# Kernel tuning notes

Measured on AMD Instinct MI355X. Metric: run time of the kernel, lower is better.

## Reference

```python
import jax, jax.numpy as jnp
import numpy as np

B, L, H, NH = 2, 512, 128, 2
DH = H // NH
POS_VOCAB, REL_VOCAB = 512, 257


def setup_inputs() -> dict:
    key = jax.random.key(0)
    ks = jax.random.split(key, 16)
    s = 0.02
    inp = {
        "query": jax.random.normal(ks[0], (B, L, H), jnp.float32),
        "key": jax.random.normal(ks[1], (B, L, H), jnp.float32),
        "value": jax.random.normal(ks[2], (B, L, H), jnp.float32),
        "Wq": jax.random.normal(ks[3], (H, H), jnp.float32) * s,
        "bq": jnp.zeros((H,), jnp.float32),
        "Wk": jax.random.normal(ks[4], (H, H), jnp.float32) * s,
        "bk": jnp.zeros((H,), jnp.float32),
        "Wv": jax.random.normal(ks[5], (H, H), jnp.float32) * s,
        "bv": jnp.zeros((H,), jnp.float32),
        "Wo": jax.random.normal(ks[6], (H, H), jnp.float32) * s,
        "bo": jnp.zeros((H,), jnp.float32),
        "E_PK": jax.random.normal(ks[7], (POS_VOCAB, H), jnp.float32) * s,
        "E_PV": jax.random.normal(ks[8], (POS_VOCAB, H), jnp.float32) * s,
        "E_RK": jax.random.normal(ks[9], (REL_VOCAB, H), jnp.float32) * s,
        "E_RV": jax.random.normal(ks[10], (REL_VOCAB, H), jnp.float32) * s,
        "poss_seq": jax.random.randint(ks[11], (B, L), 0, POS_VOCAB),
        "interval_seq": jax.random.randint(ks[12], (B, L, L), 0, REL_VOCAB),
        # causal mask (True = attend), same role as attn_mask in the torch module
        "attn_mask": jnp.broadcast_to(jnp.tril(jnp.ones((L, L), bool)), (B, L, L)),
    }
    return inp


def reference(query, key, value, Wq, bq, Wk, bk, Wv, bv, Wo, bo,
              E_PK, E_PV, E_RK, E_RV, poss_seq, interval_seq, attn_mask):
    b, l, _ = query.shape
    # linear projections (torch Linear: x @ W.T + b)
    Q = query @ Wq.T + bq
    K = key @ Wk.T + bk + E_PK[poss_seq]
    V = value @ Wv.T + bv + E_PV[poss_seq]
    # relative key/value embeddings: (b, l, l, h, dh) -> (b, h, l, l, dh)
    rel_k = E_RK[interval_seq].reshape(b, l, l, NH, DH).transpose(0, 3, 1, 2, 4)
    rel_v = E_RV[interval_seq].reshape(b, l, l, NH, DH).transpose(0, 3, 1, 2, 4)
    # split heads: (b, h, l, dh)
    Qh = Q.reshape(b, l, NH, DH).transpose(0, 2, 1, 3)
    Kh = K.reshape(b, l, NH, DH).transpose(0, 2, 1, 3)
    Vh = V.reshape(b, l, NH, DH).transpose(0, 2, 1, 3)
    scores = jnp.einsum('bhld,bhkd->bhlk', Qh, Kh)
    scores = scores + jnp.einsum('bhld,bhlkd->bhlk', Qh, rel_k)
    scores = scores / jnp.sqrt(jnp.float32(DH))
    m = attn_mask[:, None]  # (b, 1, l, l)
    scores = jnp.where(m, scores, -jnp.inf)
    w = jax.nn.softmax(scores, axis=-1)
    w = jnp.where(m, w, 0.0)
    out = jnp.einsum('bhlk,bhkd->bhld', w, Vh)
    out = out + jnp.einsum('bhlk,bhlkd->bhld', w, rel_v)
    out = out.transpose(0, 2, 1, 3).reshape(b, l, H)
    out = out @ Wo.T + bo
    out = jnp.where(jnp.isnan(out), 0.0, out)
    return out
```

## Files before the change

kernel.cpp:

```cpp
#include <hip/hip_runtime.h>
#include <math.h>

#define LL 512
#define HH 128
#define NHH 2
#define DHH 64
#define RELV 257

#define OFF_QH   0
#define OFF_KT   131072
#define OFF_VH   262144
#define OFF_PK   393216
#define OFF_WQT  919552
#define OFF_WKT  935936
#define OFF_WVT  952320
#define OFF_WOT  968704
#define OFF_ERKT 985088

__global__ void prep_kernel(const float* Wq, const float* Wk, const float* Wv,
                            const float* Wo, const float* E_RK, float* ws) {
    int g = blockIdx.x * 256 + threadIdx.x;
    if (g < 65536) {
        int m = g >> 14, rem = g & 16383, i = rem >> 7, j = rem & 127;
        const float* W = (m == 0) ? Wq : (m == 1) ? Wk : (m == 2) ? Wv : Wo;
        ws[OFF_WQT + m * 16384 + i * 128 + j] = W[j * 128 + i];
    } else if (g < 65536 + 128 * RELV) {
        int g2 = g - 65536;
        int hd = g2 / RELV, r = g2 - hd * RELV;
        ws[OFF_ERKT + hd * RELV + r] = E_RK[r * HH + hd];
    }
}

__launch_bounds__(256)
__global__ void qkv_kernel(const float* q_in, const float* k_in, const float* v_in,
                           const float* bq, const float* bk, const float* bv,
                           const float* E_PK, const float* E_PV, const int* poss,
                           const float* Wqt, const float* Wkt, const float* Wvt,
                           const float* ERKt,
                           float* Qh, float* Kt, float* Vh, float* PK) {
    int row0 = blockIdx.x * 2;
    int b = row0 >> 9;
    int l0 = row0 & 511;
    int t = threadIdx.x;

    __shared__ float xin[3][2][128];
    __shared__ float pp[3][2][2][128];
    __shared__ float qr[2][128];

    for (int g = t; g < 768; g += 256) {
        int m = g >> 8, rem = g & 255, rr = rem >> 7, i = rem & 127;
        const float* src = (m == 0) ? q_in : (m == 1) ? k_in : v_in;
        xin[m][rr][i] = src[(row0 + rr) * 128 + i];
    }
    __syncthreads();

    int j = t & 127, half = t >> 7;
    float aq0 = 0, ak0 = 0, av0 = 0, aq1 = 0, ak1 = 0, av1 = 0;
    int i0 = half * 64;
#pragma unroll 8
    for (int i = i0; i < i0 + 64; i++) {
        float wq = Wqt[i * 128 + j], wk = Wkt[i * 128 + j], wv = Wvt[i * 128 + j];
        aq0 += xin[0][0][i] * wq; aq1 += xin[0][1][i] * wq;
        ak0 += xin[1][0][i] * wk; ak1 += xin[1][1][i] * wk;
        av0 += xin[2][0][i] * wv; av1 += xin[2][1][i] * wv;
    }
    pp[0][0][half][j] = aq0; pp[0][1][half][j] = aq1;
    pp[1][0][half][j] = ak0; pp[1][1][half][j] = ak1;
    pp[2][0][half][j] = av0; pp[2][1][half][j] = av1;
    __syncthreads();

    {
        int rr = t >> 7;
        int row = row0 + rr, l = l0 + rr;
        int pos = poss[row];
        float q = pp[0][rr][0][j] + pp[0][rr][1][j] + bq[j];
        float k = pp[1][rr][0][j] + pp[1][rr][1][j] + bk[j] + E_PK[pos * 128 + j];
        float v = pp[2][rr][0][j] + pp[2][rr][1][j] + bv[j] + E_PV[pos * 128 + j];
        int h = j >> 6, d = j & 63, bh = b * NHH + h;
        Qh[(bh * LL + l) * DHH + d] = q;
        Vh[(bh * LL + l) * DHH + d] = v;
        Kt[(bh * DHH + d) * LL + l] = k;
        qr[rr][j] = q;
    }
    __syncthreads();

    int h = t >> 7, rl = t & 127;
    const float* qh0 = qr[0] + h * 64;
    const float* qh1 = qr[1] + h * 64;
    const float* erb = ERKt + h * 64 * RELV;
    float* pk0 = PK + ((b * NHH + h) * LL + l0) * RELV;
    float* pk1 = pk0 + RELV;
#pragma unroll
    for (int pass = 0; pass < 3; pass++) {
        int r = rl + pass * 128;
        if (r < RELV) {
            float a0 = 0.f, a1 = 0.f;
#pragma unroll 8
            for (int dd = 0; dd < 64; dd++) {
                float er = erb[dd * RELV + r];
                a0 += qh0[dd] * er; a1 += qh1[dd] * er;
            }
            pk0[r] = a0; pk1[r] = a1;
        }
    }
}

__launch_bounds__(512)
__global__ void attn_kernel(const float* Qh, const float* Kt, const float* Vh,
                            const float* PK, const float* E_RV,
                            const float* Wot, const float* bo,
                            const int* interval, float* out) {
    int blk = blockIdx.x;
    int b = blk & 1;
    int l = 511 - (blk >> 1);
    int t = threadIdx.x;
    int w = t >> 6, lane = t & 63;
    int h = w >> 2, s = w & 3;
    int bh = b * NHH + h;
    int nk = l + 1;
    int kstep = (((nk + 3) >> 2) + 1) & ~1;
    int kbase = s * kstep; if (kbase > nk) kbase = nk;
    int kend = kbase + kstep; if (kend > nk) kend = nk;

    __shared__ float q2[2][DHH];
    __shared__ float pks[2][RELV];
    __shared__ float wb[2][RELV];
    __shared__ __align__(8) float sc[8][128];
    __shared__ float oa[8][DHH];
    __shared__ float ao[HH];
    __shared__ float po[4][HH];
    __shared__ float reds[8];

    if (t < 128) {
        int hh = t >> 6, dd = t & 63;
        q2[hh][dd] = Qh[((b * NHH + hh) * LL + l) * DHH + dd];
    }
    for (int idx = t; idx < 2 * RELV; idx += 512) {
        int hh = idx >= RELV;
        int r = idx - hh * RELV;
        pks[hh][r] = PK[((b * NHH + hh) * LL + l) * RELV + r];
        wb[hh][r] = 0.f;
    }
    __syncthreads();

    int k0 = kbase + lane * 2;
    const int* idxr = interval + (b * LL + l) * LL;
    float ax = 0.f, ay = 0.f;
    int2 i2 = make_int2(0, 0);
    if (k0 < kend) {
        i2 = *(const int2*)(idxr + k0);
        const float* kb = Kt + bh * DHH * LL + k0;
#pragma unroll 16
        for (int d = 0; d < DHH; d++) {
            float2 kk = *(const float2*)(kb + d * LL);
            float qd = q2[h][d];
            ax += qd * kk.x; ay += qd * kk.y;
        }
    }
    float e0 = (k0 + 0 < kend) ? __expf((ax + pks[h][i2.x]) * 0.125f) : 0.f;
    float e1 = (k0 + 1 < kend) ? __expf((ay + pks[h][i2.y]) * 0.125f) : 0.f;

    float ssum = e0 + e1;
#pragma unroll
    for (int off = 32; off > 0; off >>= 1) ssum += __shfl_down(ssum, off);
    if (lane == 0) reds[w] = ssum;

    *(float2*)&sc[w][lane * 2] = make_float2(e0, e1);
    if (k0 + 0 < kend) atomicAdd(&wb[h][i2.x], e0);
    if (k0 + 1 < kend) atomicAdd(&wb[h][i2.y], e1);
    __syncthreads();

    float acc0 = 0.f, acc1 = 0.f, acc2 = 0.f, acc3 = 0.f;
    const float* vb = Vh + bh * LL * DHH + lane;
    int kcnt = kend - kbase; if (kcnt < 0) kcnt = 0;
    int niter = (kcnt + 3) >> 2;
    for (int ci = 0; ci < niter; ci++) {
        int k = kbase + ci * 4;
        const float* scw = sc[w] + ci * 4;
        acc0 += scw[0] * vb[(k + 0) * DHH];
        acc1 += scw[1] * vb[(k + 1) * DHH];
        acc2 += scw[2] * vb[(k + 2) * DHH];
        acc3 += scw[3] * vb[(k + 3) * DHH];
    }

    {
        int r0 = s * 64;
        const float* ev = E_RV + h * 64 + lane;
        const float* wbh = wb[h];
#pragma unroll 4
        for (int rr = 0; rr < 64; rr += 4) {
            int r = r0 + rr;
            acc0 += wbh[r + 0] * ev[(r + 0) * HH];
            acc1 += wbh[r + 1] * ev[(r + 1) * HH];
            acc2 += wbh[r + 2] * ev[(r + 2) * HH];
            acc3 += wbh[r + 3] * ev[(r + 3) * HH];
        }
        if (s == 3) acc0 += wbh[256] * ev[256 * HH];
    }

    float inv = 1.f / (((reds[h * 4 + 0] + reds[h * 4 + 1]) +
                        (reds[h * 4 + 2] + reds[h * 4 + 3])));
    oa[w][lane] = ((acc0 + acc1) + (acc2 + acc3)) * inv;
    __syncthreads();

    if (t < 128) {
        int hh = t >> 6, dd = t & 63;
        ao[t] = (oa[hh * 4 + 0][dd] + oa[hh * 4 + 1][dd]) +
                (oa[hh * 4 + 2][dd] + oa[hh * 4 + 3][dd]);
    }
    __syncthreads();

    int j = t & 127, iq = t >> 7;
    float pa = 0.f, pb = 0.f;
    int ib = iq * 32;
#pragma unroll 8
    for (int ii = 0; ii < 32; ii += 2) {
        pa += ao[ib + ii]     * Wot[(ib + ii) * HH + j];
        pb += ao[ib + ii + 1] * Wot[(ib + ii + 1) * HH + j];
    }
    po[iq][j] = pa + pb;
    __syncthreads();
    if (t < HH) {
        float o = (po[0][t] + po[1][t]) + (po[2][t] + po[3][t]) + bo[t];
        if (isnan(o)) o = 0.f;
        out[(b * LL + l) * HH + t] = o;
    }
}

extern "C" void kernel_launch(void* const* d_in, const int* in_sizes, int n_in,
                              void* d_out, int out_size, void* d_ws, size_t ws_size,
                              hipStream_t stream) {
    const float* query = (const float*)d_in[0];
    const float* key   = (const float*)d_in[1];
    const float* value = (const float*)d_in[2];
    const float* Wq = (const float*)d_in[3];  const float* bq = (const float*)d_in[4];
    const float* Wk = (const float*)d_in[5];  const float* bk = (const float*)d_in[6];
    const float* Wv = (const float*)d_in[7];  const float* bv = (const float*)d_in[8];
    const float* Wo = (const float*)d_in[9];  const float* bo = (const float*)d_in[10];
    const float* E_PK = (const float*)d_in[11];
    const float* E_PV = (const float*)d_in[12];
    const float* E_RK = (const float*)d_in[13];
    const float* E_RV = (const float*)d_in[14];
    const int* poss     = (const int*)d_in[15];
    const int* interval = (const int*)d_in[16];

    float* ws = (float*)d_ws;
    float* Qh   = ws + OFF_QH;
    float* Kt   = ws + OFF_KT;
    float* Vh   = ws + OFF_VH;
    float* PK   = ws + OFF_PK;
    float* Wqt  = ws + OFF_WQT;
    float* Wkt  = ws + OFF_WKT;
    float* Wvt  = ws + OFF_WVT;
    float* Wot  = ws + OFF_WOT;
    float* ERKt = ws + OFF_ERKT;
    float* out = (float*)d_out;

    prep_kernel<<<385, 256, 0, stream>>>(Wq, Wk, Wv, Wo, E_RK, ws);
    qkv_kernel<<<512, 256, 0, stream>>>(query, key, value, bq, bk, bv,
                                        E_PK, E_PV, poss, Wqt, Wkt, Wvt, ERKt,
                                        Qh, Kt, Vh, PK);
    attn_kernel<<<1024, 512, 0, stream>>>(Qh, Kt, Vh, PK, E_RV, Wot, bo,
                                          interval, out);
}
```

Measured before the change: 140.8 us.

## Fuse prep, QKV and attention kernels into one cooperative persistent kernel

Replaces the three kernel launches with one cooperative kernel that uses grid-wide syncs between the weight-transpose, projection/PK and attention phases. Blocks loop over rows persistently, with the grid sized from an occupancy query. This removes launch gaps and inter-kernel drain. In exchange it adds grid.sync overhead, a host occupancy query on every call, and a QKV phase that now handles one row per block iteration instead of two, so each weight load is reused less.

```diff
diff --git a/kernel.cpp b/kernel.cpp
--- a/kernel.cpp
+++ b/kernel.cpp
@@ -1,5 +1,8 @@
 #include <hip/hip_runtime.h>
+#include <hip/hip_cooperative_groups.h>
 #include <math.h>
+
+namespace cg = cooperative_groups;
 
 #define LL 512
 #define HH 128
@@ -17,111 +20,46 @@
 #define OFF_WOT  968704
 #define OFF_ERKT 985088
 
-__global__ void prep_kernel(const float* Wq, const float* Wk, const float* Wv,
-                            const float* Wo, const float* E_RK, float* ws) {
-    int g = blockIdx.x * 256 + threadIdx.x;
-    if (g < 65536) {
-        int m = g >> 14, rem = g & 16383, i = rem >> 7, j = rem & 127;
-        const float* W = (m == 0) ? Wq : (m == 1) ? Wk : (m == 2) ? Wv : Wo;
-        ws[OFF_WQT + m * 16384 + i * 128 + j] = W[j * 128 + i];
-    } else if (g < 65536 + 128 * RELV) {
-        int g2 = g - 65536;
-        int hd = g2 / RELV, r = g2 - hd * RELV;
-        ws[OFF_ERKT + hd * RELV + r] = E_RK[r * HH + hd];
+__global__ void fused_kernel(const float* q_in, const float* k_in, const float* v_in,
+                             const float* bq, const float* bk, const float* bv,
+                             const float* Wq, const float* Wk, const float* Wv,
+                             const float* Wo, const float* bo,
+                             const float* E_PK, const float* E_PV,
+                             const float* E_RK, const float* E_RV,
+                             const int* poss, const int* interval,
+                             float* ws, float* out) {
+    cg::grid_group grid = cg::this_grid();
+    int t = threadIdx.x;
+
+    float* Qh   = ws + OFF_QH;
+    float* Kt   = ws + OFF_KT;
+    float* Vh   = ws + OFF_VH;
+    float* PK   = ws + OFF_PK;
+    float* Wt   = ws + OFF_WQT;
+    float* ERKt = ws + OFF_ERKT;
+
+    for (int g = blockIdx.x * 512 + t; g < 65536 + 128 * RELV;
+         g += gridDim.x * 512) {
+        if (g < 65536) {
+            int m = g >> 14, rem = g & 16383, i = rem >> 7, j = rem & 127;
+            const float* W = (m == 0) ? Wq : (m == 1) ? Wk : (m == 2) ? Wv : Wo;
+            Wt[m * 16384 + i * 128 + j] = W[j * 128 + i];
+        } else {
+            int g2 = g - 65536;
+            int hd = g2 / RELV, r = g2 - hd * RELV;
+            ERKt[hd * RELV + r] = E_RK[r * HH + hd];
+        }
     }
-}
-
-__launch_bounds__(256)
-__global__ void qkv_kernel(const float* q_in, const float* k_in, const float* v_in,
-                           const float* bq, const float* bk, const float* bv,
-                           const float* E_PK, const float* E_PV, const int* poss,
-                           const float* Wqt, const float* Wkt, const float* Wvt,
-                           const float* ERKt,
-                           float* Qh, float* Kt, float* Vh, float* PK) {
-    int row0 = blockIdx.x * 2;
-    int b = row0 >> 9;
-    int l0 = row0 & 511;
-    int t = threadIdx.x;
-
-    __shared__ float xin[3][2][128];
-    __shared__ float pp[3][2][2][128];
-    __shared__ float qr[2][128];
-
-    for (int g = t; g < 768; g += 256) {
-        int m = g >> 8, rem = g & 255, rr = rem >> 7, i = rem & 127;
-        const float* src = (m == 0) ? q_in : (m == 1) ? k_in : v_in;
-        xin[m][rr][i] = src[(row0 + rr) * 128 + i];
-    }
-    __syncthreads();
-
-    int j = t & 127, half = t >> 7;
-    float aq0 = 0, ak0 = 0, av0 = 0, aq1 = 0, ak1 = 0, av1 = 0;
-    int i0 = half * 64;
-#pragma unroll 8
-    for (int i = i0; i < i0 + 64; i++) {
-        float wq = Wqt[i * 128 + j], wk = Wkt[i * 128 + j], wv = Wvt[i * 128 + j];
-        aq0 += xin[0][0][i] * wq; aq1 += xin[0][1][i] * wq;
-        ak0 += xin[1][0][i] * wk; ak1 += xin[1][1][i] * wk;
-        av0 += xin[2][0][i] * wv; av1 += xin[2][1][i] * wv;
-    }
-    pp[0][0][half][j] = aq0; pp[0][1][half][j] = aq1;
-    pp[1][0][half][j] = ak0; pp[1][1][half][j] = ak1;
-    pp[2][0][half][j] = av0; pp[2][1][half][j] = av1;
-    __syncthreads();
-
-    {
-        int rr = t >> 7;
-        int row = row0 + rr, l = l0 + rr;
-        int pos = poss[row];
-        float q = pp[0][rr][0][j] + pp[0][rr][1][j] + bq[j];
-        float k = pp[1][rr][0][j] + pp[1][rr][1][j] + bk[j] + E_PK[pos * 128 + j];
-        float v = pp[2][rr][0][j] + pp[2][rr][1][j] + bv[j] + E_PV[pos * 128 + j];
-        int h = j >> 6, d = j & 63, bh = b * NHH + h;
-        Qh[(bh * LL + l) * DHH + d] = q;
-        Vh[(bh * LL + l) * DHH + d] = v;
-        Kt[(bh * DHH + d) * LL + l] = k;
-        qr[rr][j] = q;
-    }
-    __syncthreads();
-
-    int h = t >> 7, rl = t & 127;
-    const float* qh0 = qr[0] + h * 64;
-    const float* qh1 = qr[1] + h * 64;
-    const float* erb = ERKt + h * 64 * RELV;
-    float* pk0 = PK + ((b * NHH + h) * LL + l0) * RELV;
-    float* pk1 = pk0 + RELV;
-#pragma unroll
-    for (int pass = 0; pass < 3; pass++) {
-        int r = rl + pass * 128;
-        if (r < RELV) {
-            float a0 = 0.f, a1 = 0.f;
-#pragma unroll 8
-            for (int dd = 0; dd < 64; dd++) {
-                float er = erb[dd * RELV + r];
-                a0 += qh0[dd] * er; a1 += qh1[dd] * er;
-            }
-            pk0[r] = a0; pk1[r] = a1;
-        }
-    }
-}
-
-__launch_bounds__(512)
-__global__ void attn_kernel(const float* Qh, const float* Kt, const float* Vh,
-                            const float* PK, const float* E_RV,
-                            const float* Wot, const float* bo,
-                            const int* interval, float* out) {
-    int blk = blockIdx.x;
-    int b = blk & 1;
-    int l = 511 - (blk >> 1);
-    int t = threadIdx.x;
-    int w = t >> 6, lane = t & 63;
-    int h = w >> 2, s = w & 3;
-    int bh = b * NHH + h;
-    int nk = l + 1;
-    int kstep = (((nk + 3) >> 2) + 1) & ~1;
-    int kbase = s * kstep; if (kbase > nk) kbase = nk;
-    int kend = kbase + kstep; if (kend > nk) kend = nk;
-
+    grid.sync();
+
+    const float* Wqt = Wt;
+    const float* Wkt = Wt + 16384;
+    const float* Wvt = Wt + 32768;
+    const float* Wot = Wt + 49152;
+
+    __shared__ float xin[3][128];
+    __shared__ float pp[3][4][128];
+    __shared__ float qrow[128];
     __shared__ float q2[2][DHH];
     __shared__ float pks[2][RELV];
     __shared__ float wb[2][RELV];
@@ -131,99 +69,166 @@
     __shared__ float po[4][HH];
     __shared__ float reds[8];
 
-    if (t < 128) {
-        int hh = t >> 6, dd = t & 63;
-        q2[hh][dd] = Qh[((b * NHH + hh) * LL + l) * DHH + dd];
+    for (int ri = blockIdx.x; ri < 1024; ri += gridDim.x) {
+        int b = ri & 1;
+        int l = 511 - (ri >> 1);
+        int row = b * LL + l;
+
+        if (t < 384) {
+            int m = t >> 7, i = t & 127;
+            const float* src = (m == 0) ? q_in : (m == 1) ? k_in : v_in;
+            xin[m][i] = src[row * 128 + i];
+        }
+        __syncthreads();
+
+        int j = t & 127, q4 = t >> 7;
+        float aq = 0.f, ak = 0.f, av = 0.f;
+        int i0 = q4 * 32;
+#pragma unroll 8
+        for (int i = i0; i < i0 + 32; i++) {
+            float xq = xin[0][i], xk = xin[1][i], xv = xin[2][i];
+            aq += xq * Wqt[i * 128 + j];
+            ak += xk * Wkt[i * 128 + j];
+            av += xv * Wvt[i * 128 + j];
+        }
+        pp[0][q4][j] = aq; pp[1][q4][j] = ak; pp[2][q4][j] = av;
+        __syncthreads();
+
+        if (t < 128) {
+            int pos = poss[row];
+            float q = (pp[0][0][j] + pp[0][1][j]) + (pp[0][2][j] + pp[0][3][j]) + bq[j];
+            float k = (pp[1][0][j] + pp[1][1][j]) + (pp[1][2][j] + pp[1][3][j]) + bk[j]
+                      + E_PK[pos * 128 + j];
+            float v = (pp[2][0][j] + pp[2][1][j]) + (pp[2][2][j] + pp[2][3][j]) + bv[j]
+                      + E_PV[pos * 128 + j];
+            int h = j >> 6, d = j & 63, bh = b * NHH + h;
+            Qh[(bh * LL + l) * DHH + d] = q;
+            Vh[(bh * LL + l) * DHH + d] = v;
+            Kt[(bh * DHH + d) * LL + l] = k;
+            qrow[j] = q;
+        }
+        __syncthreads();
+
+        for (int idx = t; idx < 2 * RELV; idx += 512) {
+            int h = idx >= RELV;
+            int r = idx - h * RELV;
+            const float* qh = qrow + h * 64;
+            const float* er = ERKt + h * 64 * RELV + r;
+            float acc = 0.f;
+#pragma unroll 8
+            for (int dd = 0; dd < 64; dd++) acc += qh[dd] * er[dd * RELV];
+            PK[((b * NHH + h) * LL + l) * RELV + r] = acc;
+        }
+        __syncthreads();
     }
-    for (int idx = t; idx < 2 * RELV; idx += 512) {
-        int hh = idx >= RELV;
-        int r = idx - hh * RELV;
-        pks[hh][r] = PK[((b * NHH + hh) * LL + l) * RELV + r];
-        wb[hh][r] = 0.f;
-    }
-    __syncthreads();
-
-    int k0 = kbase + lane * 2;
-    const int* idxr = interval + (b * LL + l) * LL;
-    float ax = 0.f, ay = 0.f;
-    int2 i2 = make_int2(0, 0);
-    if (k0 < kend) {
-        i2 = *(const int2*)(idxr + k0);
-        const float* kb = Kt + bh * DHH * LL + k0;
+    grid.sync();
+
+    for (int ri = blockIdx.x; ri < 1024; ri += gridDim.x) {
+        int b = ri & 1;
+        int l = 511 - (ri >> 1);
+        int w = t >> 6, lane = t & 63;
+        int h = w >> 2, s = w & 3;
+        int bh = b * NHH + h;
+        int nk = l + 1;
+        int kstep = (((nk + 3) >> 2) + 1) & ~1;
+        int kbase = s * kstep; if (kbase > nk) kbase = nk;
+        int kend = kbase + kstep; if (kend > nk) kend = nk;
+
+        if (t < 128) {
+            int hh = t >> 6, dd = t & 63;
+            q2[hh][dd] = Qh[((b * NHH + hh) * LL + l) * DHH + dd];
+        }
+        for (int idx = t; idx < 2 * RELV; idx += 512) {
+            int hh = idx >= RELV;
+            int r = idx - hh * RELV;
+            pks[hh][r] = PK[((b * NHH + hh) * LL + l) * RELV + r];
+            wb[hh][r] = 0.f;
+        }
+        __syncthreads();
+
+        int k0 = kbase + lane * 2;
+        const int* idxr = interval + (b * LL + l) * LL;
+        float ax = 0.f, ay = 0.f;
+        int2 i2 = make_int2(0, 0);
+        if (k0 < kend) {
+            i2 = *(const int2*)(idxr + k0);
+            const float* kb = Kt + bh * DHH * LL + k0;
 #pragma unroll 16
-        for (int d = 0; d < DHH; d++) {
-            float2 kk = *(const float2*)(kb + d * LL);
-            float qd = q2[h][d];
-            ax += qd * kk.x; ay += qd * kk.y;
-        }
-    }
-    float e0 = (k0 + 0 < kend) ? __expf((ax + pks[h][i2.x]) * 0.125f) : 0.f;
-    float e1 = (k0 + 1 < kend) ? __expf((ay + pks[h][i2.y]) * 0.125f) : 0.f;
-
-    float ssum = e0 + e1;
+            for (int d = 0; d < DHH; d++) {
+                float2 kk = *(const float2*)(kb + d * LL);
+                float qd = q2[h][d];
+                ax += qd * kk.x; ay += qd * kk.y;
+            }
+        }
+        float e0 = (k0 + 0 < kend) ? __expf((ax + pks[h][i2.x]) * 0.125f) : 0.f;
+        float e1 = (k0 + 1 < kend) ? __expf((ay + pks[h][i2.y]) * 0.125f) : 0.f;
+
+        float ssum = e0 + e1;
 #pragma unroll
-    for (int off = 32; off > 0; off >>= 1) ssum += __shfl_down(ssum, off);
-    if (lane == 0) reds[w] = ssum;
-
-    *(float2*)&sc[w][lane * 2] = make_float2(e0, e1);
-    if (k0 + 0 < kend) atomicAdd(&wb[h][i2.x], e0);
-    if (k0 + 1 < kend) atomicAdd(&wb[h][i2.y], e1);
-    __syncthreads();
-
-    float acc0 = 0.f, acc1 = 0.f, acc2 = 0.f, acc3 = 0.f;
-    const float* vb = Vh + bh * LL * DHH + lane;
-    int kcnt = kend - kbase; if (kcnt < 0) kcnt = 0;
-    int niter = (kcnt + 3) >> 2;
-    for (int ci = 0; ci < niter; ci++) {
-        int k = kbase + ci * 4;
-        const float* scw = sc[w] + ci * 4;
-        acc0 += scw[0] * vb[(k + 0) * DHH];
-        acc1 += scw[1] * vb[(k + 1) * DHH];
-        acc2 += scw[2] * vb[(k + 2) * DHH];
-        acc3 += scw[3] * vb[(k + 3) * DHH];
-    }
-
-    {
-        int r0 = s * 64;
-        const float* ev = E_RV + h * 64 + lane;
-        const float* wbh = wb[h];
+        for (int off = 32; off > 0; off >>= 1) ssum += __shfl_down(ssum, off);
+        if (lane == 0) reds[w] = ssum;
+
+        *(float2*)&sc[w][lane * 2] = make_float2(e0, e1);
+        if (k0 + 0 < kend) atomicAdd(&wb[h][i2.x], e0);
+        if (k0 + 1 < kend) atomicAdd(&wb[h][i2.y], e1);
+        __syncthreads();
+
+        float acc0 = 0.f, acc1 = 0.f, acc2 = 0.f, acc3 = 0.f;
+        const float* vb = Vh + bh * LL * DHH + lane;
+        int kcnt = kend - kbase; if (kcnt < 0) kcnt = 0;
+        int niter = (kcnt + 3) >> 2;
+        for (int ci = 0; ci < niter; ci++) {
+            int k = kbase + ci * 4;
+            const float* scw = sc[w] + ci * 4;
+            acc0 += scw[0] * vb[(k + 0) * DHH];
+            acc1 += scw[1] * vb[(k + 1) * DHH];
+            acc2 += scw[2] * vb[(k + 2) * DHH];
+            acc3 += scw[3] * vb[(k + 3) * DHH];
+        }
+
+        {
+            int r0 = s * 64;
+            const float* ev = E_RV + h * 64 + lane;
+            const float* wbh = wb[h];
 #pragma unroll 4
-        for (int rr = 0; rr < 64; rr += 4) {
-            int r = r0 + rr;
-            acc0 += wbh[r + 0] * ev[(r + 0) * HH];
-            acc1 += wbh[r + 1] * ev[(r + 1) * HH];
-            acc2 += wbh[r + 2] * ev[(r + 2) * HH];
-            acc3 += wbh[r + 3] * ev[(r + 3) * HH];
-        }
-        if (s == 3) acc0 += wbh[256] * ev[256 * HH];
-    }
-
-    float inv = 1.f / (((reds[h * 4 + 0] + reds[h * 4 + 1]) +
-                        (reds[h * 4 + 2] + reds[h * 4 + 3])));
-    oa[w][lane] = ((acc0 + acc1) + (acc2 + acc3)) * inv;
-    __syncthreads();
-
-    if (t < 128) {
-        int hh = t >> 6, dd = t & 63;
-        ao[t] = (oa[hh * 4 + 0][dd] + oa[hh * 4 + 1][dd]) +
-                (oa[hh * 4 + 2][dd] + oa[hh * 4 + 3][dd]);
-    }
-    __syncthreads();
-
-    int j = t & 127, iq = t >> 7;
-    float pa = 0.f, pb = 0.f;
-    int ib = iq * 32;
+            for (int rr = 0; rr < 64; rr += 4) {
+                int r = r0 + rr;
+                acc0 += wbh[r + 0] * ev[(r + 0) * HH];
+                acc1 += wbh[r + 1] * ev[(r + 1) * HH];
+                acc2 += wbh[r + 2] * ev[(r + 2) * HH];
+                acc3 += wbh[r + 3] * ev[(r + 3) * HH];
+            }
+            if (s == 3) acc0 += wbh[256] * ev[256 * HH];
+        }
+
+        float inv = 1.f / (((reds[h * 4 + 0] + reds[h * 4 + 1]) +
+                            (reds[h * 4 + 2] + reds[h * 4 + 3])));
+        oa[w][lane] = ((acc0 + acc1) + (acc2 + acc3)) * inv;
+        __syncthreads();
+
+        if (t < 128) {
+            int hh = t >> 6, dd = t & 63;
+            ao[t] = (oa[hh * 4 + 0][dd] + oa[hh * 4 + 1][dd]) +
+                    (oa[hh * 4 + 2][dd] + oa[hh * 4 + 3][dd]);
+        }
+        __syncthreads();
+
+        int j = t & 127, iq = t >> 7;
+        float pa = 0.f, pb = 0.f;
+        int ib = iq * 32;
 #pragma unroll 8
-    for (int ii = 0; ii < 32; ii += 2) {
-        pa += ao[ib + ii]     * Wot[(ib + ii) * HH + j];
-        pb += ao[ib + ii + 1] * Wot[(ib + ii + 1) * HH + j];
-    }
-    po[iq][j] = pa + pb;
-    __syncthreads();
-    if (t < HH) {
-        float o = (po[0][t] + po[1][t]) + (po[2][t] + po[3][t]) + bo[t];
-        if (isnan(o)) o = 0.f;
-        out[(b * LL + l) * HH + t] = o;
+        for (int ii = 0; ii < 32; ii += 2) {
+            pa += ao[ib + ii]     * Wot[(ib + ii) * HH + j];
+            pb += ao[ib + ii + 1] * Wot[(ib + ii + 1) * HH + j];
+        }
+        po[iq][j] = pa + pb;
+        __syncthreads();
+        if (t < HH) {
+            float o = (po[0][t] + po[1][t]) + (po[2][t] + po[3][t]) + bo[t];
+            if (isnan(o)) o = 0.f;
+            out[(b * LL + l) * HH + t] = o;
+        }
+        __syncthreads();
     }
 }
 
@@ -244,22 +249,26 @@
     const int* poss     = (const int*)d_in[15];
     const int* interval = (const int*)d_in[16];
 
-    float* ws = (float*)d_ws;
-    float* Qh   = ws + OFF_QH;
-    float* Kt   = ws + OFF_KT;
-    float* Vh   = ws + OFF_VH;
-    float* PK   = ws + OFF_PK;
-    float* Wqt  = ws + OFF_WQT;
-    float* Wkt  = ws + OFF_WKT;
-    float* Wvt  = ws + OFF_WVT;
-    float* Wot  = ws + OFF_WOT;
-    float* ERKt = ws + OFF_ERKT;
+    float* ws  = (float*)d_ws;
     float* out = (float*)d_out;
 
-    prep_kernel<<<385, 256, 0, stream>>>(Wq, Wk, Wv, Wo, E_RK, ws);
-    qkv_kernel<<<512, 256, 0, stream>>>(query, key, value, bq, bk, bv,
-                                        E_PK, E_PV, poss, Wqt, Wkt, Wvt, ERKt,
-                                        Qh, Kt, Vh, PK);
-    attn_kernel<<<1024, 512, 0, stream>>>(Qh, Kt, Vh, PK, E_RV, Wot, bo,
-                                          interval, out);
+    int blocksPerCU = 0;
+    (void)hipOccupancyMaxActiveBlocksPerMultiprocessor(&blocksPerCU,
+                                                       fused_kernel, 512, 0);
+    if (blocksPerCU < 1) blocksPerCU = 1;
+    int grid = blocksPerCU * 256;
+    if (grid > 1024) grid = 1024;
+
+    void* args[] = {
+        (void*)&query, (void*)&key, (void*)&value,
+        (void*)&bq, (void*)&bk, (void*)&bv,
+        (void*)&Wq, (void*)&Wk, (void*)&Wv,
+        (void*)&Wo, (void*)&bo,
+        (void*)&E_PK, (void*)&E_PV,
+        (void*)&E_RK, (void*)&E_RV,
+        (void*)&poss, (void*)&interval,
+        (void*)&ws, (void*)&out,
+    };
+    hipLaunchCooperativeKernel((void*)fused_kernel, dim3(grid), dim3(512),
+                               args, 0, stream);
 }
```

Result: slower. 243.4 us (+72.8%).
